# Kernel optimization log

Measured on AMD Instinct MI355X. Metric: run time of the kernel, lower is better.

## Reference

```python
import jax, jax.numpy as jnp
import numpy as np

INPUT_SIZE, HIDDEN_SIZE, OUTPUT_SIZE = 256, 512, 256
BATCH, SEQ_LEN = 64, 1024


def _xavier(key, shape):
    fan_out, fan_in = shape
    limit = float(np.sqrt(6.0 / (fan_in + fan_out)))
    return jax.random.uniform(key, shape, jnp.float32, -limit, limit)


def setup_inputs() -> dict:
    key = jax.random.key(0)
    k_x, k_w1, k_w2 = jax.random.split(key, 3)
    x = jax.random.normal(k_x, (BATCH, SEQ_LEN, INPUT_SIZE), jnp.float32)
    W_ih = _xavier(k_w1, (HIDDEN_SIZE, INPUT_SIZE + HIDDEN_SIZE))  # torch Linear weight [out, in]
    b_ih = jnp.zeros((HIDDEN_SIZE,), jnp.float32)
    W_ho = _xavier(k_w2, (OUTPUT_SIZE, HIDDEN_SIZE))
    b_ho = jnp.zeros((OUTPUT_SIZE,), jnp.float32)
    return {"x": x, "W_ih": W_ih, "b_ih": b_ih, "W_ho": W_ho, "b_ho": b_ho}


def reference(x, W_ih, b_ih, W_ho, b_ho):
    batch, seq_len, input_size = x.shape
    hidden = W_ih.shape[0]
    # Split concat-linear into two matmuls: [x_t, h] @ W^T = x_t @ Wx^T + h @ Wh^T
    Wx = W_ih[:, :input_size]   # [H, I]
    Wh = W_ih[:, input_size:]   # [H, H]
    # Precompute input projections for all timesteps: [S, B, H]
    x_proj = jnp.einsum('bsi,hi->sbh', x, Wx) + b_ih

    def step(h, xp_t):
        h_new = jnp.tanh(xp_t + h @ Wh.T)
        return h_new, h_new

    h0 = jnp.zeros((batch, hidden), x.dtype)
    _, hs = jax.lax.scan(step, h0, x_proj)          # hs: [S, B, H]
    hidden_seq = jnp.transpose(hs, (1, 0, 2))       # [B, S, H]
    final_hidden = hidden_seq[:, -1, :]             # [B, H]
    scores = jnp.einsum('bsh,bh->bs', hidden_seq, final_hidden)
    attn = jax.nn.softmax(scores, axis=1)
    context = jnp.einsum('bs,bsh->bh', attn, hidden_seq)
    return context @ W_ho.T + b_ho
```

## Files before the change

### kernel.cpp

```cpp
#include <hip/hip_runtime.h>
#include <cstdint>
#include <cmath>

#define S_LEN 1024
#define BATCH 64
#define IN_SZ 256
#define HID 512
#define OUT_SZ 256
#define WIH_LD 768
#define BH (BATCH * HID)
#define XP_FLOATS (S_LEN * BH)

#define P_REG 176
#define P_LDS 24
#define P_STR_G 14


typedef _Float16 h2v __attribute__((ext_vector_type(2)));
typedef _Float16 f16x8 __attribute__((ext_vector_type(8)));
typedef float f32x4 __attribute__((ext_vector_type(4)));

__device__ __forceinline__ float dot2p(unsigned int a, unsigned int b, float c) {
#if __has_builtin(__builtin_amdgcn_fdot2)
    return __builtin_amdgcn_fdot2(__builtin_bit_cast(h2v, a),
                                  __builtin_bit_cast(h2v, b), c, false);
#else
    h2v av = __builtin_bit_cast(h2v, a);
    h2v bv = __builtin_bit_cast(h2v, b);
    return c + (float)av.x * (float)bv.x + (float)av.y * (float)bv.y;
#endif
}

__global__ __launch_bounds__(256) void pack_w(const float* __restrict__ W_ih,
                                              unsigned int* __restrict__ wstr,
                                              unsigned int* __restrict__ wregbuf,
                                              unsigned int* __restrict__ wldsbuf) {
    int idx = blockIdx.x * 256 + threadIdx.x;
    int p = idx & 255;
    int j = idx >> 8;
    const float* src = W_ih + (size_t)j * WIH_LD + IN_SZ + 2 * p;
    unsigned short lo = __builtin_bit_cast(unsigned short, (_Float16)src[0]);
    unsigned short hi = __builtin_bit_cast(unsigned short, (_Float16)src[1]);
    unsigned int u = (unsigned int)lo | ((unsigned int)hi << 16);
    if (p < P_REG) {
        wregbuf[p * 512 + j] = u;
    } else if (p < P_REG + P_LDS) {
        wldsbuf[(p - P_REG) * 512 + j] = u;
    } else {
        int q = p - (P_REG + P_LDS);
        wstr[((q >> 2) * 512 + j) * 4 + (q & 3)] = u;
    }
}

__global__ __launch_bounds__(256) void pack_wf16(const float* __restrict__ W_ih,
                                                 uint4* __restrict__ wpk) {
    int idx = blockIdx.x * 256 + threadIdx.x;
    if (idx >= 16384) return;
    int nt   = idx >> 9;
    int ks   = (idx >> 6) & 7;
    int lane = idx & 63;
    int n  = nt * 16 + (lane & 15);
    int kb = ks * 32 + (lane >> 4) * 8;
    const float* src = W_ih + (size_t)n * WIH_LD + kb;
    union { uint4 u; _Float16 h[8]; } v;
#pragma unroll
    for (int i = 0; i < 8; ++i) v.h[i] = (_Float16)src[i];
    wpk[idx] = v.u;
}

#define AH_LD 264
__global__ __launch_bounds__(256) void xproj_mfma(const float* __restrict__ x,
                                                  const uint4* __restrict__ wpk,
                                                  const float* __restrict__ b_ih,
                                                  float* __restrict__ xp) {
    const int s    = blockIdx.x;
    const int half = blockIdx.y;
    const int tid  = threadIdx.x;
    __shared__ __align__(16) _Float16 Ah[32 * AH_LD];
    __shared__ float bsh[HID];
    bsh[tid] = b_ih[tid];
    bsh[tid + 256] = b_ih[tid + 256];
    {
        int r  = tid >> 3;
        int c0 = (tid & 7) * 32;
        const float4* s4 = (const float4*)(x + ((size_t)(half * 32 + r) * S_LEN + s) * IN_SZ + c0);
        _Float16* dst = &Ah[r * AH_LD + c0];
#pragma unroll
        for (int i = 0; i < 8; ++i) {
            float4 v = s4[i];
            dst[4 * i + 0] = (_Float16)v.x;
            dst[4 * i + 1] = (_Float16)v.y;
            dst[4 * i + 2] = (_Float16)v.z;
            dst[4 * i + 3] = (_Float16)v.w;
        }
    }
    __syncthreads();
    const int lane = tid & 63;
    const int w    = tid >> 6;
    const int mt   = w & 1;
    const int ntb  = (w >> 1) * 16;
    f16x8 areg[8];
#pragma unroll
    for (int ks = 0; ks < 8; ++ks)
        areg[ks] = *(const f16x8*)&Ah[(mt * 16 + (lane & 15)) * AH_LD + ks * 32 + (lane >> 4) * 8];
    const int brow  = half * 32 + mt * 16 + (lane >> 4) * 4;
    const int ncol0 = lane & 15;
    for (int nt2 = 0; nt2 < 16; ++nt2) {
        int nt = ntb + nt2;
        const uint4* bp = wpk + (size_t)nt * 8 * 64 + lane;
        f32x4 acc = {0.f, 0.f, 0.f, 0.f};
#pragma unroll
        for (int ks = 0; ks < 8; ++ks) {
            uint4 bu = bp[ks * 64];
            acc = __builtin_amdgcn_mfma_f32_16x16x32_f16(
                areg[ks], __builtin_bit_cast(f16x8, bu), acc, 0, 0, 0);
        }
        int n = nt * 16 + ncol0;
        float bias = bsh[n];
        float* outp = xp + (size_t)s * BH + (size_t)brow * HID + n;
#pragma unroll
        for (int r = 0; r < 4; ++r) outp[(size_t)r * HID] = acc[r] + bias;
    }
}

__global__ __launch_bounds__(512, 2) void rnn_f16(const unsigned int* __restrict__ wregbuf,
                                                  const unsigned int* __restrict__ wldsbuf,
                                                  const uint4* __restrict__ wstr,
                                                  float* __restrict__ xp) {
    const int b = blockIdx.x;
    const int j = threadIdx.x;

    __shared__ unsigned int wlds[P_LDS * 512];
    __shared__ unsigned short h2u[2][512];

    unsigned int wreg[P_REG];
#pragma unroll
    for (int p = 0; p < P_REG; ++p) wreg[p] = wregbuf[p * 512 + j];

    for (int g = j; g < P_LDS * 512; g += 512) wlds[g] = wldsbuf[g];
    h2u[0][j] = 0;
    __syncthreads();

    float* col = xp + (size_t)b * HID + j;
    for (int s = 0; s < S_LEN; ++s) {
        const unsigned int* hq = (const unsigned int*)h2u[s & 1];
        float acc = col[(size_t)s * BH];

        uint4 sw[P_STR_G];
#pragma unroll
        for (int g = 0; g < P_STR_G; ++g) sw[g] = wstr[(size_t)g * 512 + j];

#pragma unroll
        for (int p = 0; p < P_REG; ++p) acc = dot2p(wreg[p], hq[p], acc);
#pragma unroll
        for (int p = 0; p < P_LDS; ++p) acc = dot2p(wlds[p * 512 + j], hq[P_REG + p], acc);
#pragma unroll
        for (int g = 0; g < P_STR_G; ++g) {
            int pb = P_REG + P_LDS + 4 * g;
            acc = dot2p(sw[g].x, hq[pb + 0], acc);
            acc = dot2p(sw[g].y, hq[pb + 1], acc);
            acc = dot2p(sw[g].z, hq[pb + 2], acc);
            acc = dot2p(sw[g].w, hq[pb + 3], acc);
        }

        float v = tanhf(acc);
        col[(size_t)s * BH] = v;
        h2u[(s + 1) & 1][j] = __builtin_bit_cast(unsigned short, (_Float16)v);
        asm volatile("s_waitcnt lgkmcnt(0)" ::: "memory");
        asm volatile("s_barrier" ::: "memory");
    }
}

__global__ __launch_bounds__(256) void attn_sc(const float* __restrict__ hbuf,
                                               float* __restrict__ sc_g) {
    const int b     = blockIdx.x;
    const int chunk = blockIdx.y;
    const int tid   = threadIdx.x;
    const int lane  = tid & 63;
    const int wv    = tid >> 6;
    __shared__ float fh[HID];
    fh[tid] = hbuf[(size_t)(S_LEN - 1) * BH + (size_t)b * HID + tid];
    fh[tid + 256] = hbuf[(size_t)(S_LEN - 1) * BH + (size_t)b * HID + tid + 256];
    __syncthreads();
    float4 f0 = *(const float4*)&fh[lane * 8];
    float4 f1 = *(const float4*)&fh[lane * 8 + 4];
    for (int i = 0; i < 32; ++i) {
        int s = chunk * 128 + wv * 32 + i;
        const float* hr = hbuf + (size_t)s * BH + (size_t)b * HID + lane * 8;
        float4 a0 = *(const float4*)hr;
        float4 a1 = *(const float4*)(hr + 4);
        float p = a0.x * f0.x + a0.y * f0.y + a0.z * f0.z + a0.w * f0.w +
                  a1.x * f1.x + a1.y * f1.y + a1.z * f1.z + a1.w * f1.w;
#pragma unroll
        for (int off = 32; off; off >>= 1) p += __shfl_down(p, off, 64);
        if (lane == 0) sc_g[(size_t)b * S_LEN + s] = p;
    }
}

__global__ __launch_bounds__(256) void attn_ctx(const float* __restrict__ hbuf,
                                                const float* __restrict__ sc_g,
                                                float* __restrict__ ctx_g) {
    const int b   = blockIdx.x;
    const int hc  = blockIdx.y * 128;
    const int tid = threadIdx.x;
    const int lane = tid & 63;
    const int wv   = tid >> 6;
    __shared__ float sc[S_LEN];
    __shared__ float red[4];
    __shared__ float part[256];
    for (int i = tid; i < S_LEN; i += 256) sc[i] = sc_g[(size_t)b * S_LEN + i];
    __syncthreads();
    float m = -1e30f;
    for (int i = tid; i < S_LEN; i += 256) m = fmaxf(m, sc[i]);
#pragma unroll
    for (int off = 32; off; off >>= 1) m = fmaxf(m, __shfl_down(m, off, 64));
    if (lane == 0) red[wv] = m;
    __syncthreads();
    m = fmaxf(fmaxf(red[0], red[1]), fmaxf(red[2], red[3]));
    float sum = 0.f;
    for (int i = tid; i < S_LEN; i += 256) {
        float e = __expf(sc[i] - m);
        sc[i] = e;
        sum += e;
    }
#pragma unroll
    for (int off = 32; off; off >>= 1) sum += __shfl_down(sum, off, 64);
    __syncthreads();
    if (lane == 0) red[wv] = sum;
    __syncthreads();
    float inv = 1.f / (red[0] + red[1] + red[2] + red[3]);
    const int h  = hc + (tid & 127);
    const int sh = tid >> 7;
    const float* hp = hbuf + (size_t)sh * 512 * BH + (size_t)b * HID + h;
    float c = 0.f;
#pragma unroll 4
    for (int s2 = 0; s2 < 512; ++s2)
        c += sc[sh * 512 + s2] * hp[(size_t)s2 * BH];
    part[tid] = c;
    __syncthreads();
    if (tid < 128) ctx_g[(size_t)b * HID + hc + tid] = (part[tid] + part[tid + 128]) * inv;
}

__global__ __launch_bounds__(256) void attn_fin(const float* __restrict__ ctx_g,
                                                const float* __restrict__ W_ho,
                                                const float* __restrict__ b_ho,
                                                float* __restrict__ out) {
    const int b   = blockIdx.x;
    const int tid = threadIdx.x;
    __shared__ float ctx[HID];
    ctx[tid] = ctx_g[(size_t)b * HID + tid];
    ctx[tid + 256] = ctx_g[(size_t)b * HID + tid + 256];
    __syncthreads();
    float o = b_ho[tid];
    const float* wr = W_ho + (size_t)tid * HID;
#pragma unroll 4
    for (int k = 0; k < HID; ++k) o += wr[k] * ctx[k];
    out[(size_t)b * OUT_SZ + tid] = o;
}

extern "C" void kernel_launch(void* const* d_in, const int* in_sizes, int n_in,
                              void* d_out, int out_size, void* d_ws, size_t ws_size,
                              hipStream_t stream) {
    const float* x    = (const float*)d_in[0];
    const float* W_ih = (const float*)d_in[1];
    const float* b_ih = (const float*)d_in[2];
    const float* W_ho = (const float*)d_in[3];
    const float* b_ho = (const float*)d_in[4];
    float* out = (float*)d_out;
    float* ws  = (float*)d_ws;

    float* xp = ws;
    unsigned int* wbase   = (unsigned int*)(ws + XP_FLOATS);
    unsigned int* wstr    = wbase;
    unsigned int* wregbuf = wbase + 28672;
    unsigned int* wldsbuf = wbase + 28672 + P_REG * 512;
    uint4*        wpk     = (uint4*)(wbase + 131072);
    float*        sc_g    = (float*)wbase;
    float*        ctx_g   = (float*)(wbase + 65536);

    pack_w<<<dim3(512), dim3(256), 0, stream>>>(W_ih, wstr, wregbuf, wldsbuf);
    pack_wf16<<<dim3(64), dim3(256), 0, stream>>>(W_ih, wpk);
    xproj_mfma<<<dim3(1024, 2), dim3(256), 0, stream>>>(x, wpk, b_ih, xp);
    rnn_f16<<<dim3(64), dim3(512), 0, stream>>>(wregbuf, wldsbuf, (const uint4*)wstr, xp);
    attn_sc<<<dim3(64, 8), dim3(256), 0, stream>>>(xp, sc_g);
    attn_ctx<<<dim3(64, 4), dim3(256), 0, stream>>>(xp, sc_g, ctx_g);
    attn_fin<<<dim3(64), dim3(256), 0, stream>>>(ctx_g, W_ho, b_ho, out);
}
```

Baseline: 1.959 ms.

## Replace per-batch fdot2 recurrence with MFMA recurrence over 16-row batch tiles

The recurrent step is rewritten from one block per batch row doing scalar fp16 dot2 products into 4 blocks, each processing 16 batch rows with MFMA 16x16x32 instructions. The hidden-to-hidden weights are repacked into MFMA B-fragment layout. Most fragments stay in registers, some sit in LDS, and the last k-tile is streamed from global memory each step. This trades 64 parallel blocks for 4 blocks that make heavier use of the matrix cores, which cuts total work per step but uses far fewer CUs and keeps a long serial chain.

```diff
diff --git a/kernel.cpp b/kernel.cpp
--- a/kernel.cpp
+++ b/kernel.cpp
@@ -11,45 +11,23 @@
 #define BH (BATCH * HID)
 #define XP_FLOATS (S_LEN * BH)
 
-#define P_REG 176
-#define P_LDS 24
-#define P_STR_G 14
-
-
-typedef _Float16 h2v __attribute__((ext_vector_type(2)));
+
 typedef _Float16 f16x8 __attribute__((ext_vector_type(8)));
 typedef float f32x4 __attribute__((ext_vector_type(4)));
 
-__device__ __forceinline__ float dot2p(unsigned int a, unsigned int b, float c) {
-#if __has_builtin(__builtin_amdgcn_fdot2)
-    return __builtin_amdgcn_fdot2(__builtin_bit_cast(h2v, a),
-                                  __builtin_bit_cast(h2v, b), c, false);
-#else
-    h2v av = __builtin_bit_cast(h2v, a);
-    h2v bv = __builtin_bit_cast(h2v, b);
-    return c + (float)av.x * (float)bv.x + (float)av.y * (float)bv.y;
-#endif
-}
-
-__global__ __launch_bounds__(256) void pack_w(const float* __restrict__ W_ih,
-                                              unsigned int* __restrict__ wstr,
-                                              unsigned int* __restrict__ wregbuf,
-                                              unsigned int* __restrict__ wldsbuf) {
-    int idx = blockIdx.x * 256 + threadIdx.x;
-    int p = idx & 255;
-    int j = idx >> 8;
-    const float* src = W_ih + (size_t)j * WIH_LD + IN_SZ + 2 * p;
-    unsigned short lo = __builtin_bit_cast(unsigned short, (_Float16)src[0]);
-    unsigned short hi = __builtin_bit_cast(unsigned short, (_Float16)src[1]);
-    unsigned int u = (unsigned int)lo | ((unsigned int)hi << 16);
-    if (p < P_REG) {
-        wregbuf[p * 512 + j] = u;
-    } else if (p < P_REG + P_LDS) {
-        wldsbuf[(p - P_REG) * 512 + j] = u;
-    } else {
-        int q = p - (P_REG + P_LDS);
-        wstr[((q >> 2) * 512 + j) * 4 + (q & 3)] = u;
-    }
+__global__ __launch_bounds__(256) void pack_whB(const float* __restrict__ W_ih,
+                                                uint4* __restrict__ whB) {
+    int idx  = blockIdx.x * 256 + threadIdx.x;
+    int lane = idx & 63;
+    int kt   = (idx >> 6) & 15;
+    int nt   = idx >> 10;
+    int n = nt * 16 + (lane & 15);
+    int k = kt * 32 + ((lane >> 4) << 3);
+    const float* src = W_ih + (size_t)n * WIH_LD + IN_SZ + k;
+    union { uint4 u; _Float16 h[8]; } v;
+#pragma unroll
+    for (int i = 0; i < 8; ++i) v.h[i] = (_Float16)src[i];
+    whB[idx] = v.u;
 }
 
 __global__ __launch_bounds__(256) void pack_wf16(const float* __restrict__ W_ih,
@@ -123,49 +101,73 @@
     }
 }
 
-__global__ __launch_bounds__(512, 2) void rnn_f16(const unsigned int* __restrict__ wregbuf,
-                                                  const unsigned int* __restrict__ wldsbuf,
-                                                  const uint4* __restrict__ wstr,
-                                                  float* __restrict__ xp) {
-    const int b = blockIdx.x;
-    const int j = threadIdx.x;
-
-    __shared__ unsigned int wlds[P_LDS * 512];
-    __shared__ unsigned short h2u[2][512];
-
-    unsigned int wreg[P_REG];
-#pragma unroll
-    for (int p = 0; p < P_REG; ++p) wreg[p] = wregbuf[p * 512 + j];
-
-    for (int g = j; g < P_LDS * 512; g += 512) wlds[g] = wldsbuf[g];
-    h2u[0][j] = 0;
-    __syncthreads();
-
-    float* col = xp + (size_t)b * HID + j;
+__global__ __launch_bounds__(256, 1) void rnn_mfma(const uint4* __restrict__ whB,
+                                                   float* __restrict__ xp) {
+    const int g    = blockIdx.x;
+    const int tid  = threadIdx.x;
+    const int lane = tid & 63;
+    const int w    = tid >> 6;
+
+    __shared__ uint4 Blds[4 * 8 * 3 * 64];
+    __shared__ __align__(16) _Float16 hA[2][16][520];
+
+    const uint4* bw = whB + (size_t)w * 8192 + lane;
+
+    f16x8 Breg[96];
+#pragma unroll
+    for (int ntl = 0; ntl < 8; ++ntl)
+#pragma unroll
+        for (int kt = 0; kt < 12; ++kt)
+            Breg[ntl * 12 + kt] = __builtin_bit_cast(f16x8, bw[(ntl * 16 + kt) * 64]);
+
+#pragma unroll
+    for (int ntl = 0; ntl < 8; ++ntl)
+#pragma unroll
+        for (int q = 0; q < 3; ++q)
+            Blds[((w * 8 + ntl) * 3 + q) * 64 + lane] = bw[(ntl * 16 + 12 + q) * 64];
+
+    for (int t = tid; t < 16 * 520; t += 256) ((_Float16*)hA[0])[t] = (_Float16)0.f;
+    __syncthreads();
+
+    const int mr   = (lane >> 4) << 2;
+    const int ncol = w * 128 + (lane & 15);
     for (int s = 0; s < S_LEN; ++s) {
-        const unsigned int* hq = (const unsigned int*)h2u[s & 1];
-        float acc = col[(size_t)s * BH];
-
-        uint4 sw[P_STR_G];
-#pragma unroll
-        for (int g = 0; g < P_STR_G; ++g) sw[g] = wstr[(size_t)g * 512 + j];
-
-#pragma unroll
-        for (int p = 0; p < P_REG; ++p) acc = dot2p(wreg[p], hq[p], acc);
-#pragma unroll
-        for (int p = 0; p < P_LDS; ++p) acc = dot2p(wlds[p * 512 + j], hq[P_REG + p], acc);
-#pragma unroll
-        for (int g = 0; g < P_STR_G; ++g) {
-            int pb = P_REG + P_LDS + 4 * g;
-            acc = dot2p(sw[g].x, hq[pb + 0], acc);
-            acc = dot2p(sw[g].y, hq[pb + 1], acc);
-            acc = dot2p(sw[g].z, hq[pb + 2], acc);
-            acc = dot2p(sw[g].w, hq[pb + 3], acc);
+        const int par = s & 1;
+        float* xs = xp + (size_t)s * BH + (size_t)(g * 16 + mr) * HID + ncol;
+        float xpv[8][4];
+#pragma unroll
+        for (int ntl = 0; ntl < 8; ++ntl)
+#pragma unroll
+            for (int r = 0; r < 4; ++r)
+                xpv[ntl][r] = xs[(size_t)r * HID + ntl * 16];
+        f16x8 sw[8];
+#pragma unroll
+        for (int ntl = 0; ntl < 8; ++ntl)
+            sw[ntl] = __builtin_bit_cast(f16x8, bw[(ntl * 16 + 15) * 64]);
+
+        f32x4 acc[8] = {};
+#pragma unroll
+        for (int kt = 0; kt < 16; ++kt) {
+            f16x8 aF = *(const f16x8*)&hA[par][lane & 15][kt * 32 + (lane >> 4) * 8];
+#pragma unroll
+            for (int ntl = 0; ntl < 8; ++ntl) {
+                f16x8 bF = (kt < 12)
+                             ? Breg[ntl * 12 + kt]
+                             : (kt < 15)
+                                 ? __builtin_bit_cast(f16x8,
+                                       Blds[((w * 8 + ntl) * 3 + (kt - 12)) * 64 + lane])
+                                 : sw[ntl];
+                acc[ntl] = __builtin_amdgcn_mfma_f32_16x16x32_f16(aF, bF, acc[ntl], 0, 0, 0);
+            }
         }
-
-        float v = tanhf(acc);
-        col[(size_t)s * BH] = v;
-        h2u[(s + 1) & 1][j] = __builtin_bit_cast(unsigned short, (_Float16)v);
+#pragma unroll
+        for (int ntl = 0; ntl < 8; ++ntl)
+#pragma unroll
+            for (int r = 0; r < 4; ++r) {
+                float v = tanhf(acc[ntl][r] + xpv[ntl][r]);
+                xs[(size_t)r * HID + ntl * 16] = v;
+                hA[par ^ 1][mr + r][ncol + ntl * 16] = (_Float16)v;
+            }
         asm volatile("s_waitcnt lgkmcnt(0)" ::: "memory");
         asm volatile("s_barrier" ::: "memory");
     }
@@ -270,18 +272,16 @@
     float* ws  = (float*)d_ws;
 
     float* xp = ws;
-    unsigned int* wbase   = (unsigned int*)(ws + XP_FLOATS);
-    unsigned int* wstr    = wbase;
-    unsigned int* wregbuf = wbase + 28672;
-    unsigned int* wldsbuf = wbase + 28672 + P_REG * 512;
-    uint4*        wpk     = (uint4*)(wbase + 131072);
-    float*        sc_g    = (float*)wbase;
-    float*        ctx_g   = (float*)(wbase + 65536);
-
-    pack_w<<<dim3(512), dim3(256), 0, stream>>>(W_ih, wstr, wregbuf, wldsbuf);
+    unsigned int* wbase = (unsigned int*)(ws + XP_FLOATS);
+    uint4* whB   = (uint4*)wbase;
+    uint4* wpk   = (uint4*)(wbase + 131072);
+    float* sc_g  = (float*)wbase;
+    float* ctx_g = (float*)(wbase + 65536);
+
+    pack_whB<<<dim3(128), dim3(256), 0, stream>>>(W_ih, whB);
     pack_wf16<<<dim3(64), dim3(256), 0, stream>>>(W_ih, wpk);
     xproj_mfma<<<dim3(1024, 2), dim3(256), 0, stream>>>(x, wpk, b_ih, xp);
-    rnn_f16<<<dim3(64), dim3(512), 0, stream>>>(wregbuf, wldsbuf, (const uint4*)wstr, xp);
+    rnn_mfma<<<dim3(4), dim3(256), 0, stream>>>(whB, xp);
     attn_sc<<<dim3(64, 8), dim3(256), 0, stream>>>(xp, sc_g);
     attn_ctx<<<dim3(64, 4), dim3(256), 0, stream>>>(xp, sc_g, ctx_g);
     attn_fin<<<dim3(64), dim3(256), 0, stream>>>(ctx_g, W_ho, b_ho, out);
```

New measurement: 5.280 ms. 170% more time.
